# Kernel tuning notes

Measured on AMD Instinct MI355X. Metric: run time of the kernel, lower is better.

Reference implementation:

```python
import math
import jax, jax.numpy as jnp
import numpy as np

B, N, QN, LN = 2, 2048, 512, 256
D, QD, LD = 1024, 1024, 64
H, QH = 16, 16
HD, QHD = D // H, QD // QH


def setup_inputs() -> dict:
    key = jax.random.key(0)
    ks = jax.random.split(key, 12)
    g = lambda k, shp, s: (jax.random.normal(k, shp, dtype=jnp.float32) * s)
    return {
        "x": g(ks[0], (B, N, D), 1.0),
        "query": g(ks[1], (B, QN, QD), 1.0),
        "low_res": g(ks[2], (B, LN, LD), 1.0),
        "W_qkv": g(ks[3], (D, 3 * D), 0.02),          # self.qkv (no bias)
        "W_xkv": g(ks[4], (D, 2 * QD), 0.02),         # self.x_to_query_kv
        "W_qlin": g(ks[5], (QD, 3 * QD), 0.02),       # self.query_linear
        "gate": g(ks[6], (1, QH, 1, 1), 0.5),         # self.gate
        "W_proj": g(ks[7], (D, D), 0.02),
        "b_proj": jnp.zeros((D,), jnp.float32),
        "W_qproj": g(ks[8], (QD, QD), 0.02),
        "b_qproj": jnp.zeros((QD,), jnp.float32),
        "W_lrproj": g(ks[9], (LD, LD), 0.02),
        "b_lrproj": jnp.zeros((LD,), jnp.float32),
    }


def _sdpa(q, k, v):
    # q,k,v: [B, H, S, hd]; plain softmax attention, no mask, no dropout
    scale = 1.0 / math.sqrt(q.shape[-1])
    attn = jax.nn.softmax(jnp.einsum("bhqd,bhkd->bhqk", q, k) * scale, axis=-1)
    return jnp.einsum("bhqk,bhkd->bhqd", attn, v)


def reference(x, query, low_res, W_qkv, W_xkv, W_qlin, gate,
              W_proj, b_proj, W_qproj, b_qproj, W_lrproj, b_lrproj):
    # --- self-attention over x ---
    qkv = (x @ W_qkv).reshape(B, N, 3, H, HD).transpose(2, 0, 3, 1, 4)
    q, k, v = qkv[0], qkv[1], qkv[2]          # [B,H,N,HD]
    x_attn = _sdpa(q, k, v)                    # [B,H,N,HD]

    # --- zero_init gated cross-attention for query stream ---
    kv = (x @ W_xkv).reshape(B, N, 2, QH, QHD).transpose(2, 0, 3, 1, 4)
    k2, v2 = kv[0], kv[1]                      # [B,QH,N,QHD]
    qqkv = (query @ W_qlin).reshape(B, QN, 3, QH, QHD).transpose(2, 0, 3, 1, 4)
    qq, qk, qv = qqkv[0], qqkv[1], qqkv[2]     # [B,QH,QN,QHD]

    xk = jnp.concatenate([k2, qk], axis=2)     # [B,QH,N+QN,QHD]
    xv = jnp.concatenate([v2, qv], axis=2)
    scale = 1.0 / math.sqrt(QHD)
    scores = jnp.einsum("bhqd,bhkd->bhqk", qq, xk) * scale  # [B,QH,QN,N+QN]
    # split softmax with learned tanh gate on the x segment
    attn = jnp.concatenate(
        [jnp.tanh(gate) * jax.nn.softmax(scores[..., :N], axis=-1),
         jax.nn.softmax(scores[..., N:], axis=-1)], axis=-1)
    q_attn = jnp.einsum("bhqk,bhkd->bhqd", attn, xv)  # [B,QH,QN,QHD]

    # --- output projections ---
    x_out = x_attn.transpose(0, 2, 1, 3).reshape(B, N, D) @ W_proj + b_proj
    query_out = q_attn.transpose(0, 2, 1, 3).reshape(B, QN, QD) @ W_qproj + b_qproj
    # faithful to source: low_res passes through unmodified in zero_init branch,
    # then transpose(1,2)+reshape scramble, then proj
    lr_out = jnp.swapaxes(low_res, 1, 2).reshape(B, LN, LD) @ W_lrproj + b_lrproj
    return (x_out, query_out, lr_out)
```

## Files before the change

### kernel.cpp

```cpp
#include <hip/hip_runtime.h>

typedef __bf16 bf16;
typedef __bf16 bf16x4 __attribute__((ext_vector_type(4)));
typedef __bf16 bf16x8 __attribute__((ext_vector_type(8)));
typedef float  f32x4  __attribute__((ext_vector_type(4)));


#define AS1(p) ((const __attribute__((address_space(1))) void*)(p))
#define AS3(p) ((__attribute__((address_space(3))) void*)(p))
__device__ __forceinline__ void gl16(const void* g, void* l) {
    __builtin_amdgcn_global_load_lds(AS1(g), AS3(l), 16, 0, 0);
}
#define BAR_VM4() asm volatile("s_waitcnt vmcnt(4)\n\ts_barrier" ::: "memory")
#define BAR_VM2() asm volatile("s_waitcnt vmcnt(2)\n\ts_barrier" ::: "memory")
#define BAR_VM0() asm volatile("s_waitcnt vmcnt(0)\n\ts_barrier" ::: "memory")
#define BAR()     asm volatile("s_barrier" ::: "memory")

__global__ __launch_bounds__(256) void cast_bf16(
    const float* __restrict__ s0, bf16* __restrict__ d0, int n0,
    const float* __restrict__ s1, bf16* __restrict__ d1, int n1)
{
    int idx = (blockIdx.x * 256 + threadIdx.x) << 3;
    const float* s; bf16* d;
    if (idx < n0) { s = s0 + idx; d = d0 + idx; }
    else { int k = idx - n0; if (k >= n1) return; s = s1 + k; d = d1 + k; }
    f32x4 a = *(const f32x4*)s, c = *(const f32x4*)(s + 4);
    bf16x8 v;
#pragma unroll
    for (int j = 0; j < 4; j++) { v[j] = (bf16)a[j]; v[4 + j] = (bf16)c[j]; }
    *(bf16x8*)d = v;
}

__global__ __launch_bounds__(256) void wtrans(
    const float* __restrict__ S0, bf16* __restrict__ D0,
    const float* __restrict__ S1, bf16* __restrict__ D1,
    const float* __restrict__ S2, bf16* __restrict__ D2,
    const float* __restrict__ S3, bf16* __restrict__ D3,
    const float* __restrict__ S4, bf16* __restrict__ D4)
{
    __shared__ float T[64][65];
    int gx = blockIdx.x, k0 = blockIdx.y << 6;
    const float* S; bf16* D; int N;
    if (gx < 48)       { S = S0; D = D0; N = 3072; }
    else if (gx < 80)  { S = S1; D = D1; N = 2048; gx -= 48; }
    else if (gx < 128) { S = S2; D = D2; N = 3072; gx -= 80; }
    else if (gx < 144) { S = S3; D = D3; N = 1024; gx -= 128; }
    else               { S = S4; D = D4; N = 1024; gx -= 144; }
    int n0 = gx << 6, tid = threadIdx.x;
#pragma unroll
    for (int rr = 0; rr < 4; rr++) {
        int row = (rr << 4) + (tid >> 4), col = (tid & 15) << 2;
        f32x4 v = *(const f32x4*)(S + (size_t)(k0 + row) * N + n0 + col);
#pragma unroll
        for (int j = 0; j < 4; j++) T[col + j][row] = v[j];
    }
    __syncthreads();
    {
        int n = tid >> 2, kc = (tid & 3) << 4;
        bf16x8 v0, v1;
#pragma unroll
        for (int j = 0; j < 8; j++) {
            v0[j] = (bf16)T[n][kc + j];
            v1[j] = (bf16)T[n][kc + 8 + j];
        }
        bf16* dp = D + (size_t)(n0 + n) * 1024 + k0 + kc;
        *(bf16x8*)dp = v0; *(bf16x8*)(dp + 8) = v1;
    }
}

template <int NSPLIT, typename OT>
__global__ __launch_bounds__(256) void gemm_bt(
    const bf16* __restrict__ A, const bf16* __restrict__ Bt,
    OT* __restrict__ C0, OT* __restrict__ C1, OT* __restrict__ C2,
    OT* __restrict__ C3, OT* __restrict__ C4,
    const float* __restrict__ bias, int M, int N, int K, int tshift,
    float s0scale, unsigned vmask)
{
    __shared__ __align__(16) bf16 gsm[18432];

    const int tid  = threadIdx.x;
    const int wave = tid >> 6, lane = tid & 63;
    const int l15  = lane & 15, g = lane >> 4;
    const int wr   = wave & 1, wc = wave >> 1;
    const int m0   = blockIdx.y << 7, n0 = blockIdx.x << 7;

    f32x4 acc[4][4] = {};

    auto stage = [&](int t, int bsel) {
        const bf16* Ab = A  + (size_t)m0 * K + (t << 5);
        const bf16* Bb = Bt + (size_t)n0 * K + (t << 5);
        char* Ad = (char*)gsm + (bsel << 14);
        char* Bd = Ad + 8192;
        const int wb = (tid & 192) << 4;
#pragma unroll
        for (int i = 0; i < 2; i++) {
            int L = (i << 8) + tid;
            int r = L >> 2, c = (L & 3) ^ ((r ^ (r >> 2)) & 3);
            gl16(Ab + (size_t)r * K + (c << 3), Ad + (i << 12) + wb);
            gl16(Bb + (size_t)r * K + (c << 3), Bd + (i << 12) + wb);
        }
    };
    auto compute = [&](int bsel) {
        const char* Ad = (const char*)gsm + (bsel << 14);
        const char* Bd = Ad + 8192;
        bf16x8 af[4], bq[4];
#pragma unroll
        for (int mb = 0; mb < 4; mb++) {
            int row = (wr << 6) + (mb << 4) + l15;
            af[mb] = *(const bf16x8*)(Ad + (row << 6)
                      + ((g ^ ((row ^ (row >> 2)) & 3)) << 4));
        }
#pragma unroll
        for (int nb = 0; nb < 4; nb++) {
            int row = (wc << 6) + (nb << 4) + l15;
            bq[nb] = *(const bf16x8*)(Bd + (row << 6)
                      + ((g ^ ((row ^ (row >> 2)) & 3)) << 4));
        }
#pragma unroll
        for (int mb = 0; mb < 4; mb++)
#pragma unroll
            for (int nb = 0; nb < 4; nb++)
                acc[mb][nb] = __builtin_amdgcn_mfma_f32_16x16x32_bf16(
                    af[mb], bq[nb], acc[mb][nb], 0, 0, 0);
    };

    const int T = K >> 5;
    stage(0, 0);
    for (int t = 0; t < T; t++) {
        int bsel = t & 1;
        if (t + 1 < T) { stage(t + 1, bsel ^ 1); BAR_VM4(); }
        else           { BAR_VM0(); }
        compute(bsel);
        BAR();
    }

    if constexpr (NSPLIT == 0) {
#pragma unroll
        for (int mb = 0; mb < 4; mb++)
#pragma unroll
            for (int nb = 0; nb < 4; nb++) {
                int n = n0 + (wc << 6) + (nb << 4) + l15;
                int mbase = m0 + (wr << 6) + (mb << 4) + (g << 2);
                float bi = bias[n];
#pragma unroll
                for (int r = 0; r < 4; r++)
                    C0[(size_t)(mbase + r) * N + n] = (OT)(acc[mb][nb][r] + bi);
            }
    } else {
        BAR();
        bf16* stg = gsm + wave * 4608;
        const int nh = (n0 >> 6) + wc;
        const int sl = nh >> 4, hq = nh & 15;
        const float scl = (sl == 0) ? s0scale : 1.0f;
        const bool isv = (vmask >> sl) & 1;
        if (isv) {
#pragma unroll
            for (int mb = 0; mb < 4; mb++)
#pragma unroll
                for (int nb = 0; nb < 4; nb++)
#pragma unroll
                    for (int r = 0; r < 4; r++)
                        stg[((nb << 4) + l15) * 72 + (mb << 4) + (g << 2) + r]
                            = (bf16)(acc[mb][nb][r] * scl);
        } else {
#pragma unroll
            for (int mb = 0; mb < 4; mb++)
#pragma unroll
                for (int nb = 0; nb < 4; nb++)
#pragma unroll
                    for (int r = 0; r < 4; r++)
                        stg[((mb << 4) + (g << 2) + r) << 6 | ((nb << 4) + l15)]
                            = (bf16)(acc[mb][nb][r] * scl);
        }
        __syncthreads();
        const int ntok = 1 << tshift;
        const int tok0 = m0 + (wr << 6);
        const int b = tok0 >> tshift, t0 = tok0 & (ntok - 1);
        const int bh_ = (b << 4) + hq;
        OT* dst = (sl == 0) ? C0 : (sl == 1) ? C1 : (sl == 2) ? C2
                : (sl == 3) ? C3 : C4;
#pragma unroll
        for (int rr = 0; rr < 8; rr++) {
            int idx = (rr << 6) + lane;
            int rowi = idx >> 3, c = idx & 7;
            if (isv) {
                bf16x8 vv = *(const bf16x8*)&stg[rowi * 72 + (c << 3)];
                *(bf16x8*)&dst[((size_t)((bh_ << 6) + rowi)) * ntok + t0 + (c << 3)] = vv;
            } else {
                bf16x8 vv = *(const bf16x8*)&stg[(rowi << 6) + (c << 3)];
                *(bf16x8*)&dst[(((size_t)bh_ * ntok + t0 + rowi) << 6) + (c << 3)] = vv;
            }
        }
    }
}

__global__ __launch_bounds__(256) void flash3m(
    const bf16* __restrict__ Q1, const bf16* __restrict__ K1,
    const bf16* __restrict__ V1t, bf16* __restrict__ O1,
    const bf16* __restrict__ Q2, const bf16* __restrict__ K2a,
    const bf16* __restrict__ V2at, const bf16* __restrict__ K2b,
    const bf16* __restrict__ V2bt, bf16* __restrict__ O2,
    const float* __restrict__ gate)
{
    __shared__ __align__(16) bf16 fsm[12288];

    const int tid = threadIdx.x;
    const int wave = tid >> 6, lane = tid & 63;
    const int l15 = lane & 15, g = lane >> 4;

    const int j = blockIdx.x & 7, i = blockIdx.x >> 3;
    const bf16 *Qp, *Ka, *Vat, *Kb2, *Vbt2; bf16* Op;
    int nq, nk1, nk2, q0, bh;
    bool cross;
    if (i < 16) {
        cross = true;
        bh = (j << 2) + (i >> 2); q0 = (i & 3) << 7;
        Qp = Q2; Ka = K2a; Vat = V2at; Kb2 = K2b; Vbt2 = V2bt; Op = O2;
        nq = 512; nk1 = 2048; nk2 = 512;
    } else {
        cross = false;
        int is = i - 16;
        bh = (j << 2) + (is >> 4); q0 = (is & 15) << 7;
        Qp = Q1; Ka = K1; Vat = V1t; Kb2 = nullptr; Vbt2 = nullptr; Op = O1;
        nq = 2048; nk1 = 2048; nk2 = 0;
    }
    const int h = bh & 15, b = bh >> 4;
    const int T1 = nk1 >> 5, T = T1 + (cross ? (nk2 >> 5) : 0);
    const int swzc = (l15 ^ (l15 >> 2)) & 3;

    char* Psw = (char*)fsm + 16384 + (wave << 11);

    bf16x8 qf[2][2];
#pragma unroll
    for (int qb = 0; qb < 2; qb++) {
        const bf16* qrow = Qp + ((size_t)bh * nq + q0 + (wave << 5) + (qb << 4) + l15) * 64;
        qf[qb][0] = *(const bf16x8*)(qrow + (g << 3));
        qf[qb][1] = *(const bf16x8*)(qrow + 32 + (g << 3));
    }

    f32x4 Oacc[4][2] = {}, Ofin[4][2] = {};
    float lcur[2] = {0.0f, 0.0f};
    const float gmul = cross ? tanhf(gate[h]) : 1.0f;

    auto stage = [&](int t, int bsel) {
        const bf16 *kb, *vb; int stride;
        if (!cross || t < T1) {
            kb = Ka + ((size_t)bh * nk1 + (t << 5)) * 64;
            vb = Vat + ((size_t)bh << 6) * nk1 + (t << 5);
            stride = nk1;
        } else {
            int u = t - T1;
            kb = Kb2 + ((size_t)bh * nk2 + (u << 5)) * 64;
            vb = Vbt2 + ((size_t)bh << 6) * nk2 + (u << 5);
            stride = nk2;
        }
        char* Kd = (char*)fsm + (bsel << 12);
        char* Vd = (char*)fsm + 8192 + (bsel << 12);
        const int wb = (tid & 192) << 4;
        {
            int r = tid >> 3, c = (tid & 7) ^ (r & 7);
            gl16(kb + (r << 6) + (c << 3), Kd + wb);
        }
        {
            int r = tid >> 2, c = (tid & 3) ^ (r & 3);
            gl16(vb + (size_t)r * stride + (c << 3), Vd + wb);
        }
    };

    auto compute = [&](int t, int bsel) {
        const char* Kb = (const char*)fsm + (bsel << 12);
        const char* Vb = (const char*)fsm + 8192 + (bsel << 12);
        f32x4 S[2][2];
#pragma unroll
        for (int nb = 0; nb < 2; nb++) {
            int row = (nb << 4) + l15;
            bf16x8 kf0 = *(const bf16x8*)(Kb + (row << 7) + ((g ^ (row & 7)) << 4));
            bf16x8 kf1 = *(const bf16x8*)(Kb + (row << 7) + (((4 + g) ^ (row & 7)) << 4));
#pragma unroll
            for (int qb = 0; qb < 2; qb++) {
                f32x4 s = {};
                s = __builtin_amdgcn_mfma_f32_16x16x32_bf16(kf0, qf[qb][0], s, 0, 0, 0);
                s = __builtin_amdgcn_mfma_f32_16x16x32_bf16(kf1, qf[qb][1], s, 0, 0, 0);
                S[nb][qb] = s;
            }
        }
        float rs[2] = {0.0f, 0.0f};
#pragma unroll
        for (int qb = 0; qb < 2; qb++)
#pragma unroll
            for (int nb = 0; nb < 2; nb++) {
                bf16x4 pv;
#pragma unroll
                for (int r = 0; r < 4; r++) {
                    float p = __builtin_amdgcn_exp2f(S[nb][qb][r]);
                    rs[qb] += p;
                    pv[r] = (bf16)p;
                }
                *(bf16x4*)(Psw + (((qb << 4) + l15) << 6)
                    + ((((nb << 1) + (g >> 1)) ^ swzc) << 4) + ((g & 1) << 3)) = pv;
            }
#pragma unroll
        for (int qb = 0; qb < 2; qb++) {
            rs[qb] += __shfl_xor(rs[qb], 16);
            rs[qb] += __shfl_xor(rs[qb], 32);
            lcur[qb] += rs[qb];
        }
        bf16x8 pf[2];
#pragma unroll
        for (int qb = 0; qb < 2; qb++)
            pf[qb] = *(const bf16x8*)(Psw + (((qb << 4) + l15) << 6)
                          + ((g ^ swzc) << 4));
#pragma unroll
        for (int hb = 0; hb < 4; hb++) {
            int row = (hb << 4) + l15;
            bf16x8 vf = *(const bf16x8*)(Vb + (row << 6) + ((g ^ (row & 3)) << 4));
#pragma unroll
            for (int qb = 0; qb < 2; qb++)
                Oacc[hb][qb] = __builtin_amdgcn_mfma_f32_16x16x32_bf16(
                    vf, pf[qb], Oacc[hb][qb], 0, 0, 0);
        }
        if (cross && t == T1 - 1) {
#pragma unroll
            for (int qb = 0; qb < 2; qb++) {
                float w = gmul / lcur[qb];
#pragma unroll
                for (int hb = 0; hb < 4; hb++)
#pragma unroll
                    for (int r = 0; r < 4; r++) {
                        Ofin[hb][qb][r] += Oacc[hb][qb][r] * w;
                        Oacc[hb][qb][r] = 0.0f;
                    }
                lcur[qb] = 0.0f;
            }
        }
    };

    stage(0, 0);
    for (int t = 0; t < T; t++) {
        int bsel = t & 1;
        if (t + 1 < T) { stage(t + 1, bsel ^ 1); BAR_VM2(); }
        else           { BAR_VM0(); }
        compute(t, bsel);
        BAR();
    }

    float wfin[2];
#pragma unroll
    for (int qb = 0; qb < 2; qb++)
        wfin[qb] = (cross ? 1.0f : gmul) / lcur[qb];

    bf16* OB = fsm;
#pragma unroll
    for (int hb = 0; hb < 4; hb++)
#pragma unroll
        for (int qb = 0; qb < 2; qb++)
#pragma unroll
            for (int r = 0; r < 4; r++) {
                float v = Oacc[hb][qb][r] * wfin[qb];
                if (cross) v += Ofin[hb][qb][r];
                OB[((hb << 4) + (g << 2) + r) * 136 + (wave << 5) + (qb << 4) + l15] = (bf16)v;
            }
    __syncthreads();
    {
        int q = tid >> 1, half = (tid & 1) << 5;
        bf16x8 o[4];
#pragma unroll
        for (int j2 = 0; j2 < 4; j2++)
#pragma unroll
            for (int jj = 0; jj < 8; jj++)
                o[j2][jj] = OB[(half + (j2 << 3) + jj) * 136 + q];
        bf16* op = Op + (((size_t)b * nq + q0 + q) << 10) + (h << 6) + half;
#pragma unroll
        for (int j2 = 0; j2 < 4; j2++)
            *(bf16x8*)(op + (j2 << 3)) = o[j2];
    }
}

__global__ __launch_bounds__(256) void lr_kernel(
    const float* __restrict__ low_res, const float* __restrict__ W,
    const float* __restrict__ bias, float* __restrict__ out)
{
    int idx = blockIdx.x * 256 + threadIdx.x;
    int j = idx & 63, i = (idx >> 6) & 255, b = idx >> 14;
    float acc = bias[j];
    const float* lr = low_res + ((size_t)b << 14);
    for (int k = 0; k < 64; k++) {
        int f = i * 64 + k;
        acc += lr[((f & 255) << 6) + (f >> 8)] * W[(k << 6) + j];
    }
    out[idx] = acc;
}

extern "C" void kernel_launch(void* const* d_in, const int* in_sizes, int n_in,
                              void* d_out, int out_size, void* d_ws, size_t ws_size,
                              hipStream_t stream)
{
    const float* x       = (const float*)d_in[0];
    const float* query   = (const float*)d_in[1];
    const float* lowres  = (const float*)d_in[2];
    const float* W_qkv   = (const float*)d_in[3];
    const float* W_xkv   = (const float*)d_in[4];
    const float* W_qlin  = (const float*)d_in[5];
    const float* gate    = (const float*)d_in[6];
    const float* W_proj  = (const float*)d_in[7];
    const float* b_proj  = (const float*)d_in[8];
    const float* W_qproj = (const float*)d_in[9];
    const float* b_qproj = (const float*)d_in[10];
    const float* W_lr    = (const float*)d_in[11];
    const float* b_lr    = (const float*)d_in[12];
    float* out = (float*)d_out;

    const float sc2 = 0.125f * 1.44269504088896f;

    char* ws = (char*)d_ws;
    bf16* WtX     = (bf16*)ws; ws += 10485760;
    bf16* Wtqlin  = (bf16*)ws; ws += 6291456;
    bf16* Wtproj  = (bf16*)ws; ws += 2097152;
    bf16* Wtqproj = (bf16*)ws; ws += 2097152;
    bf16* xb      = (bf16*)ws; ws += 8388608;
    bf16* qryb    = (bf16*)ws; ws += 2097152;
    bf16* qb      = (bf16*)ws; ws += 8388608;
    bf16* kb      = (bf16*)ws; ws += 8388608;
    bf16* vbt     = (bf16*)ws; ws += 8388608;
    bf16* k2      = (bf16*)ws; ws += 8388608;
    bf16* v2t     = (bf16*)ws; ws += 8388608;
    bf16* qq      = (bf16*)ws; ws += 2097152;
    bf16* qk      = (bf16*)ws; ws += 2097152;
    bf16* qvt     = (bf16*)ws; ws += 2097152;
    bf16* ax = xb;
    bf16* aq = qryb;

    cast_bf16<<<2560, 256, 0, stream>>>(x, xb, 4194304, query, qryb, 1048576);
    wtrans<<<dim3(160, 16), 256, 0, stream>>>(
        W_qkv, WtX, W_xkv, WtX + (size_t)3072 * 1024,
        W_qlin, Wtqlin, W_proj, Wtproj, W_qproj, Wtqproj);

    gemm_bt<5, bf16><<<dim3(40, 32), 256, 0, stream>>>(
        xb, WtX, qb, kb, vbt, k2, v2t, nullptr, 4096, 5120, 1024, 11, sc2, 0b10100u);
    gemm_bt<3, bf16><<<dim3(24, 8), 256, 0, stream>>>(
        qryb, Wtqlin, qq, qk, qvt, nullptr, nullptr, nullptr, 1024, 3072, 1024, 9, sc2, 0b100u);

    flash3m<<<640, 256, 0, stream>>>(
        qb, kb, vbt, ax, qq, k2, v2t, qk, qvt, aq, gate);

    gemm_bt<0, float><<<dim3(8, 32), 256, 0, stream>>>(
        ax, Wtproj, out, nullptr, nullptr, nullptr, nullptr, b_proj,
        4096, 1024, 1024, 0, 1.0f, 0u);
    gemm_bt<0, float><<<dim3(8, 8), 256, 0, stream>>>(
        aq, Wtqproj, out + 4194304, nullptr, nullptr, nullptr, nullptr, b_qproj,
        1024, 1024, 1024, 0, 1.0f, 0u);
    lr_kernel<<<128, 256, 0, stream>>>(lowres, W_lr, b_lr, out + 5242880);

    (void)in_sizes; (void)n_in; (void)out_size; (void)ws_size;
}
```

Before: 323.0 us.

## Permute V-transpose layout so softmax probabilities feed PV MFMA from registers

The QKV GEMM epilogue now writes transposed V with a permuted token order inside each 32-token block. That order matches the register layout of the QK^T MFMA output, so the flash kernel can pack exp2 probabilities straight into the B operand of the PV MFMA. This drops the per-tile LDS write and read of P along with its swizzle, and shrinks shared memory. The per-tile cross-lane row-sum shuffles move to one reduction at each normalization point. The cost is split 8-byte global stores in the epilogue instead of 16-byte ones, plus a hidden layout contract between the two kernels.

```diff
diff --git a/kernel.cpp b/kernel.cpp
--- a/kernel.cpp
+++ b/kernel.cpp
@@ -185,7 +185,15 @@
             int rowi = idx >> 3, c = idx & 7;
             if (isv) {
                 bf16x8 vv = *(const bf16x8*)&stg[rowi * 72 + (c << 3)];
-                *(bf16x8*)&dst[((size_t)((bh_ << 6) + rowi)) * ntok + t0 + (c << 3)] = vv;
+                bf16x4 lo, hi;
+#pragma unroll
+                for (int jj = 0; jj < 4; jj++) { lo[jj] = vv[jj]; hi[jj] = vv[4 + jj]; }
+                int tb = t0 + ((c >> 2) << 5);
+                int gamma0 = (c << 1) & 7;
+                int p_lo = (((gamma0 & 3) << 1) + (gamma0 >> 2)) << 2;
+                size_t base = ((size_t)((bh_ << 6) + rowi)) * ntok + tb;
+                *(bf16x4*)&dst[base + p_lo] = lo;
+                *(bf16x4*)&dst[base + p_lo + 8] = hi;
             } else {
                 bf16x8 vv = *(const bf16x8*)&stg[(rowi << 6) + (c << 3)];
                 *(bf16x8*)&dst[(((size_t)bh_ * ntok + t0 + rowi) << 6) + (c << 3)] = vv;
@@ -202,7 +210,7 @@
     const bf16* __restrict__ V2bt, bf16* __restrict__ O2,
     const float* __restrict__ gate)
 {
-    __shared__ __align__(16) bf16 fsm[12288];
+    __shared__ __align__(16) bf16 fsm[8704];
 
     const int tid = threadIdx.x;
     const int wave = tid >> 6, lane = tid & 63;
@@ -226,9 +234,6 @@
     }
     const int h = bh & 15, b = bh >> 4;
     const int T1 = nk1 >> 5, T = T1 + (cross ? (nk2 >> 5) : 0);
-    const int swzc = (l15 ^ (l15 >> 2)) & 3;
-
-    char* Psw = (char*)fsm + 16384 + (wave << 11);
 
     bf16x8 qf[2][2];
 #pragma unroll
@@ -284,32 +289,20 @@
                 S[nb][qb] = s;
             }
         }
-        float rs[2] = {0.0f, 0.0f};
-#pragma unroll
-        for (int qb = 0; qb < 2; qb++)
-#pragma unroll
-            for (int nb = 0; nb < 2; nb++) {
-                bf16x4 pv;
-#pragma unroll
-                for (int r = 0; r < 4; r++) {
-                    float p = __builtin_amdgcn_exp2f(S[nb][qb][r]);
-                    rs[qb] += p;
-                    pv[r] = (bf16)p;
-                }
-                *(bf16x4*)(Psw + (((qb << 4) + l15) << 6)
-                    + ((((nb << 1) + (g >> 1)) ^ swzc) << 4) + ((g & 1) << 3)) = pv;
-            }
+        bf16x8 pf[2];
 #pragma unroll
         for (int qb = 0; qb < 2; qb++) {
-            rs[qb] += __shfl_xor(rs[qb], 16);
-            rs[qb] += __shfl_xor(rs[qb], 32);
-            lcur[qb] += rs[qb];
-        }
-        bf16x8 pf[2];
-#pragma unroll
-        for (int qb = 0; qb < 2; qb++)
-            pf[qb] = *(const bf16x8*)(Psw + (((qb << 4) + l15) << 6)
-                          + ((g ^ swzc) << 4));
+            float rs = 0.0f;
+#pragma unroll
+            for (int r = 0; r < 4; r++) {
+                float p0 = __builtin_amdgcn_exp2f(S[0][qb][r]);
+                float p1 = __builtin_amdgcn_exp2f(S[1][qb][r]);
+                rs += p0 + p1;
+                pf[qb][r] = (bf16)p0;
+                pf[qb][4 + r] = (bf16)p1;
+            }
+            lcur[qb] += rs;
+        }
 #pragma unroll
         for (int hb = 0; hb < 4; hb++) {
             int row = (hb << 4) + l15;
@@ -322,7 +315,10 @@
         if (cross && t == T1 - 1) {
 #pragma unroll
             for (int qb = 0; qb < 2; qb++) {
-                float w = gmul / lcur[qb];
+                float l = lcur[qb];
+                l += __shfl_xor(l, 16);
+                l += __shfl_xor(l, 32);
+                float w = gmul / l;
 #pragma unroll
                 for (int hb = 0; hb < 4; hb++)
 #pragma unroll
@@ -346,8 +342,12 @@
 
     float wfin[2];
 #pragma unroll
-    for (int qb = 0; qb < 2; qb++)
-        wfin[qb] = (cross ? 1.0f : gmul) / lcur[qb];
+    for (int qb = 0; qb < 2; qb++) {
+        float l = lcur[qb];
+        l += __shfl_xor(l, 16);
+        l += __shfl_xor(l, 32);
+        wfin[qb] = 1.0f / l;
+    }
 
     bf16* OB = fsm;
 #pragma unroll
```

Result: faster. 309.5 us (-4.2%).
